# Kernel optimization log

Measured on AMD Instinct MI355X. Metric: run time of the kernel, lower is better.

The kernel has to match this reference:

```python
import jax, jax.numpy as jnp
import numpy as np

K = 4  # kNN neighbors


def build_edges(density_maps, k):
    B, _, H, W = density_maps.shape
    N = H * W
    flat = density_maps.reshape(B, N)
    # [B, N, N] pairwise absolute density distance
    dist = jnp.abs(flat[:, :, None] - flat[:, None, :])
    # k nearest (excluding self at position 0)
    tgt = jnp.argsort(dist, axis=2)[:, :, 1:k + 1]  # [B, N, k]
    src = jnp.broadcast_to(jnp.arange(N)[None, :, None], (B, N, k))
    offset = (jnp.arange(B) * N)[:, None, None]
    src = (src + offset).reshape(-1)
    tgt = (tgt + offset).reshape(-1)
    n_total = B * N
    loops = jnp.arange(n_total)
    row = jnp.concatenate([src, loops])  # source nodes
    col = jnp.concatenate([tgt, loops])  # target nodes
    return row, col, n_total


def gcn_conv(x, row, col, W, b, n_nodes):
    # symmetric deg^-1/2 normalization, deg computed on target (col)
    deg = jax.ops.segment_sum(jnp.ones_like(col, dtype=x.dtype), col, num_segments=n_nodes)
    dinv = jnp.where(deg > 0, jax.lax.rsqrt(deg), 0.0)
    norm = dinv[row] * dinv[col]  # [E]
    h = x @ W  # transform first, then propagate
    msg = norm[:, None] * h[row]
    out = jax.ops.segment_sum(msg, col, num_segments=n_nodes)
    return out + b


def setup_inputs() -> dict:
    key = jax.random.key(0)
    k1, k2, k3, k4, k5, k6 = jax.random.split(key, 6)
    B, Cin, Chid, Cout, H, W = 4, 256, 512, 256, 64, 64
    density_maps = jax.random.uniform(k1, (B, 1, H, W), dtype=jnp.float32)
    feature_maps = jax.random.normal(k2, (B, Cin, H, W), dtype=jnp.float32)
    W1 = jax.random.normal(k3, (Cin, Chid), dtype=jnp.float32) * (1.0 / np.sqrt(Cin))
    b1 = jnp.zeros((Chid,), dtype=jnp.float32)
    W2 = jax.random.normal(k4, (Chid, Cout), dtype=jnp.float32) * (1.0 / np.sqrt(Chid))
    b2 = jnp.zeros((Cout,), dtype=jnp.float32)
    return {"density_maps": density_maps, "feature_maps": feature_maps,
            "W1": W1, "b1": b1, "W2": W2, "b2": b2}


def reference(density_maps, feature_maps, W1, b1, W2, b2):
    B, Cin, H, Wd = feature_maps.shape
    row, col, n_total = build_edges(density_maps, K)
    # [B,C,H,W] -> [B*H*W, C] node features
    x = feature_maps.transpose(0, 2, 3, 1).reshape(-1, Cin)
    h = jax.nn.relu(gcn_conv(x, row, col, W1, b1, n_total))
    out = jax.nn.relu(gcn_conv(h, row, col, W2, b2, n_total))
    return out.reshape(B, H, Wd, -1).transpose(0, 3, 1, 2)
```

## Files before the change

### kernel.cpp

```cpp
#include <hip/hip_runtime.h>
#include <hip/hip_bf16.h>
#include <stdint.h>

#define N_NODES 16384
#define NPB     4096
#define NB      4
#define KNN     4
#define WIN     12
#define NBUK    4096

typedef short bf16x8 __attribute__((ext_vector_type(8)));
typedef float f32x4 __attribute__((ext_vector_type(4)));
typedef unsigned short u16x8 __attribute__((ext_vector_type(8)));

__device__ __forceinline__ unsigned short f2bf(float f) {
  unsigned u = __float_as_uint(f);
  unsigned r = (u + 0x7fff + ((u >> 16) & 1)) >> 16;
  return (unsigned short)r;
}
__device__ __forceinline__ float bf2f(unsigned short u) {
  return __uint_as_float(((unsigned)u) << 16);
}

__global__ __launch_bounds__(1024)
void bucket_kernel(const float* __restrict__ dm,
                   unsigned long long* __restrict__ skeys_g,
                   int* __restrict__ rank_g,
                   int* __restrict__ deg_g,
                   unsigned* __restrict__ mask_g) {
  __shared__ int sHist[4096];
  __shared__ int sCur[4096];
  __shared__ unsigned long long sKeys[4096];
  int* part1 = (int*)sKeys;
  int* part2 = (int*)(sKeys + 512);
  const int t = threadIdx.x, b = blockIdx.x;
  const float* d = dm + b * NPB;

  unsigned long long kv[4]; int bk[4];
#pragma unroll
  for (int r = 0; r < 4; ++r) sHist[t + r * 1024] = 0;
  __syncthreads();
#pragma unroll
  for (int r = 0; r < 4; ++r) {
    int i = t + r * 1024;
    float v = d[i];
    kv[r] = (((unsigned long long)__float_as_uint(v)) << 32) | (unsigned)i;
    int k = (int)(v * (float)NBUK); if (k > NBUK - 1) k = NBUK - 1;
    bk[r] = k;
    atomicAdd(&sHist[k], 1);
  }
  __syncthreads();
  int c0 = sHist[4 * t + 0], c1 = sHist[4 * t + 1];
  int c2 = sHist[4 * t + 2], c3 = sHist[4 * t + 3];
  part1[t] = c0 + c1 + c2 + c3;
  __syncthreads();
  if (t < 64) {
    int s = 0;
#pragma unroll
    for (int k = 0; k < 16; ++k) s += part1[16 * t + k];
    part2[t] = s;
  }
  __syncthreads();
  if (t == 0) {
    int a = 0;
    for (int u = 0; u < 64; ++u) { int v = part2[u]; part2[u] = a; a += v; }
  }
  __syncthreads();
  int base = part2[t >> 4];
  for (int k = (t >> 4) * 16; k < t; ++k) base += part1[k];
  sHist[4 * t + 0] = base; sCur[4 * t + 0] = base; base += c0;
  sHist[4 * t + 1] = base; sCur[4 * t + 1] = base; base += c1;
  sHist[4 * t + 2] = base; sCur[4 * t + 2] = base; base += c2;
  sHist[4 * t + 3] = base; sCur[4 * t + 3] = base;
  __syncthreads();
#pragma unroll
  for (int r = 0; r < 4; ++r) {
    int slot = atomicAdd(&sCur[bk[r]], 1);
    sKeys[slot] = kv[r];
  }
  __syncthreads();
#pragma unroll
  for (int r = 0; r < 4; ++r) {
    int g = t + r * 1024;
    int s0 = sHist[g];
    int s1 = (g == NPB - 1) ? NPB : sHist[g + 1];
    for (int i = s0 + 1; i < s1; ++i) {
      unsigned long long x = sKeys[i];
      int j = i - 1;
      while (j >= s0 && sKeys[j] > x) { sKeys[j + 1] = sKeys[j]; --j; }
      sKeys[j + 1] = x;
    }
  }
  __syncthreads();
#pragma unroll
  for (int r = 0; r < 4; ++r) {
    int i = t + r * 1024;
    unsigned long long k = sKeys[i];
    skeys_g[b * NPB + i] = k;
    rank_g[b * NPB + (int)(k & 0xffffffffull)] = i;
    deg_g[b * NPB + i] = 1;
    mask_g[b * NPB + i] = 0;
  }
}

__global__ void select_kernel(const unsigned long long* __restrict__ skeys,
                              int* __restrict__ deg, unsigned* __restrict__ mask) {
  int p = blockIdx.x * 256 + threadIdx.x;
  if (p >= N_NODES) return;
  int b = p >> 12, pl = p & (NPB - 1);
  const unsigned long long* sk = skeys + b * NPB;
  unsigned long long kp = sk[pl];
  float di = __uint_as_float((unsigned)(kp >> 32));
  int lo = pl - WIN; if (lo < 0) lo = 0;
  int hi = pl + WIN; if (hi > NPB - 1) hi = NPB - 1;
  unsigned long long k0 = ~0ull, k1 = ~0ull, k2 = ~0ull, k3 = ~0ull, k4 = ~0ull;
  for (int q = lo; q <= hi; ++q) {
    unsigned long long key = sk[q];
    float v = __uint_as_float((unsigned)(key >> 32));
    float dist = fabsf(di - v);
    unsigned long long dk = (((unsigned long long)__float_as_uint(dist)) << 24) |
                            ((key & 0xfffull) << 12) | (unsigned)q;
    if (dk < k4) {
      if (dk < k0)      { k4 = k3; k3 = k2; k2 = k1; k1 = k0; k0 = dk; }
      else if (dk < k1) { k4 = k3; k3 = k2; k2 = k1; k1 = dk; }
      else if (dk < k2) { k4 = k3; k3 = k2; k2 = dk; }
      else if (dk < k3) { k4 = k3; k3 = dk; }
      else              { k4 = dk; }
    }
  }
  int base = b * NPB;
  int t0 = (int)(k1 & 0xfff), t1 = (int)(k2 & 0xfff);
  int t2 = (int)(k3 & 0xfff), t3 = (int)(k4 & 0xfff);
  atomicAdd(&deg[base + t0], 1); atomicOr(&mask[base + t0], 1u << (pl - t0 + WIN));
  atomicAdd(&deg[base + t1], 1); atomicOr(&mask[base + t1], 1u << (pl - t1 + WIN));
  atomicAdd(&deg[base + t2], 1); atomicOr(&mask[base + t2], 1u << (pl - t2 + WIN));
  atomicAdd(&deg[base + t3], 1); atomicOr(&mask[base + t3], 1u << (pl - t3 + WIN));
}

__global__ void cvt_all_kernel(const float* __restrict__ fm, unsigned short* __restrict__ px0,
                               const float* __restrict__ W1, unsigned short* __restrict__ W1t,
                               const float* __restrict__ W2, unsigned short* __restrict__ W2t,
                               const int* __restrict__ rank) {
  __shared__ float tile[64][33];
  int z = blockIdx.z;
  const float* in; unsigned short* outbase; int Rin, Cin, r0, c0;
  bool perm = false;
  if (z < NB) {
    in = fm + (size_t)z * 256 * 4096; outbase = px0 + (size_t)z * NPB * 256;
    Rin = 256; Cin = 4096; perm = true;
    c0 = blockIdx.x * 32; r0 = blockIdx.y * 64;
  } else {
    int id = blockIdx.y * 128 + blockIdx.x;
    if (id < 64)       { in = W1; outbase = W1t; Rin = 256; Cin = 512; c0 = (id & 15) * 32; r0 = (id >> 4) * 64; }
    else if (id < 128) { id -= 64; in = W2; outbase = W2t; Rin = 512; Cin = 256; c0 = (id & 7) * 32; r0 = (id >> 3) * 64; }
    else return;
  }
  int tx = threadIdx.x & 31, ty = threadIdx.x >> 5;
  const float* ip = in + (size_t)(r0 + ty) * Cin + c0 + tx;
#pragma unroll
  for (int i = 0; i < 8; ++i) tile[ty + 8 * i][tx] = ip[(size_t)(8 * i) * Cin];
  __syncthreads();
  int orow = threadIdx.x >> 3;
  int oseg = (threadIdx.x & 7) * 8;
  int outrow = c0 + orow;
  if (perm) outrow = rank[(size_t)z * NPB + outrow];
  unsigned short* op = outbase + (size_t)outrow * Rin + r0 + oseg;
  u16x8 o;
#pragma unroll
  for (int k = 0; k < 8; ++k) o[k] = f2bf(tile[oseg + k][orow]);
  *(u16x8*)op = o;
}

__global__ __launch_bounds__(256)
void transpose64_kernel(const float* __restrict__ in, float* __restrict__ out) {
  __shared__ float tile[64][68];
  int cb = blockIdx.x * 64;
  int nb = blockIdx.y * 64;
  int b = blockIdx.z;
  int r = threadIdx.x >> 2, q = threadIdx.x & 3;
  const float* ip = in + ((size_t)b * NPB + nb + r) * 256 + cb;
#pragma unroll
  for (int it = 0; it < 4; ++it) {
    int c = q * 4 + it * 16;
    *(float4*)&tile[r][c] = *(const float4*)(ip + c);
  }
  __syncthreads();
  float* op = out + ((size_t)b * 256 + cb + r) * 4096 + nb;
#pragma unroll
  for (int it = 0; it < 4; ++it) {
    int n = q * 4 + it * 16;
    float4 v;
    v.x = tile[n + 0][r]; v.y = tile[n + 1][r];
    v.z = tile[n + 2][r]; v.w = tile[n + 3][r];
    *(float4*)(op + n) = v;
  }
}

__global__ void prop_kernel(const unsigned short* __restrict__ in,
                            unsigned short* __restrict__ out,
                            const unsigned* __restrict__ mask,
                            const int* __restrict__ deg) {
  int i = blockIdx.x * 8 + (threadIdx.x >> 5);
  int l = threadIdx.x & 31;
  unsigned m = mask[i];
  float a[8] = {};
#pragma unroll
  for (int off = 0; off < 2 * WIN + 1; ++off) {
    int c = ((m >> off) & 1) + (off == WIN);
    if (c) {
      int q = i + off - WIN;
      float dj = (float)c * rsqrtf((float)deg[q]);
      u16x8 u = *(const u16x8*)(in + (size_t)q * 256 + l * 8);
#pragma unroll
      for (int k = 0; k < 8; ++k) a[k] = fmaf(dj, bf2f(u[k]), a[k]);
    }
  }
  float di = rsqrtf((float)deg[i]);
  u16x8 o;
#pragma unroll
  for (int k = 0; k < 8; ++k) o[k] = f2bf(a[k] * di);
  *(u16x8*)(out + (size_t)i * 256 + l * 8) = o;
}

__global__ void prop2_kernel(const unsigned short* __restrict__ in,
                             float* __restrict__ out,
                             const unsigned* __restrict__ mask,
                             const int* __restrict__ deg,
                             const float* __restrict__ bias,
                             const unsigned long long* __restrict__ skeys) {
  int i = blockIdx.x * 8 + (threadIdx.x >> 5);
  int l = threadIdx.x & 31;
  unsigned m = mask[i];
  float a[8] = {};
#pragma unroll
  for (int off = 0; off < 2 * WIN + 1; ++off) {
    int c = ((m >> off) & 1) + (off == WIN);
    if (c) {
      int q = i + off - WIN;
      float dj = (float)c * rsqrtf((float)deg[q]);
      u16x8 u = *(const u16x8*)(in + (size_t)q * 256 + l * 8);
#pragma unroll
      for (int k = 0; k < 8; ++k) a[k] = fmaf(dj, bf2f(u[k]), a[k]);
    }
  }
  float di = rsqrtf((float)deg[i]);
  int node = (i & ~(NPB - 1)) + (int)(skeys[i] & 0xffffffffull);
  float4 o0, o1;
  o0.x = fmaxf(a[0] * di + bias[l * 8 + 0], 0.f);
  o0.y = fmaxf(a[1] * di + bias[l * 8 + 1], 0.f);
  o0.z = fmaxf(a[2] * di + bias[l * 8 + 2], 0.f);
  o0.w = fmaxf(a[3] * di + bias[l * 8 + 3], 0.f);
  o1.x = fmaxf(a[4] * di + bias[l * 8 + 4], 0.f);
  o1.y = fmaxf(a[5] * di + bias[l * 8 + 5], 0.f);
  o1.z = fmaxf(a[6] * di + bias[l * 8 + 6], 0.f);
  o1.w = fmaxf(a[7] * di + bias[l * 8 + 7], 0.f);
  *(float4*)(out + (size_t)node * 256 + l * 8) = o0;
  *(float4*)(out + (size_t)node * 256 + l * 8 + 4) = o1;
}

template <bool BIAS_RELU, bool OUT_BF16, int NI>
__global__ __launch_bounds__(256)
void gemm_bf16_kernel(const unsigned short* __restrict__ A,
                      const unsigned short* __restrict__ Bt,
                      void* __restrict__ C, const float* __restrict__ bias,
                      int M, int N, int K) {
  __shared__ char lds[8192 + NI * 8192];
  const int tid = threadIdx.x;
  const int l = tid & 63, w = tid >> 6;
  const int bm = blockIdx.x * 64, bn = blockIdx.y * (64 * NI);
  f32x4 acc[4][NI] = {};

  for (int k0 = 0; k0 < K; k0 += 64) {
    __syncthreads();
#pragma unroll
    for (int q = 0; q < 2; ++q) {
      int o = q * 4096 + tid * 16;
      int r = o >> 7;
      int gc = ((o >> 4) & 7) ^ (r & 7);
      const char* srcA = (const char*)A + ((size_t)(bm + r) * K + k0) * 2 + gc * 16;
      __builtin_amdgcn_global_load_lds(
          (const __attribute__((address_space(1))) void*)srcA,
          (__attribute__((address_space(3))) void*)(lds + o), 16, 0, 0);
    }
#pragma unroll
    for (int q = 0; q < 2 * NI; ++q) {
      int o = q * 4096 + tid * 16;
      int r = o >> 7;
      int gc = ((o >> 4) & 7) ^ (r & 7);
      const char* srcB = (const char*)Bt + ((size_t)(bn + r) * K + k0) * 2 + gc * 16;
      __builtin_amdgcn_global_load_lds(
          (const __attribute__((address_space(1))) void*)srcB,
          (__attribute__((address_space(3))) void*)(lds + 8192 + o), 16, 0, 0);
    }
    __syncthreads();

#pragma unroll
    for (int kk = 0; kk < 64; kk += 32) {
      bf16x8 af[4], bf[NI];
      int gc = (kk >> 3) + (l >> 4);
#pragma unroll
      for (int mi = 0; mi < 4; ++mi) {
        int r = mi * 16 + (l & 15);
        af[mi] = *(const bf16x8*)(lds + r * 128 + ((gc ^ (r & 7)) << 4));
      }
#pragma unroll
      for (int ni = 0; ni < NI; ++ni) {
        int r = w * (16 * NI) + ni * 16 + (l & 15);
        bf[ni] = *(const bf16x8*)(lds + 8192 + r * 128 + ((gc ^ (r & 7)) << 4));
      }
#pragma unroll
      for (int mi = 0; mi < 4; ++mi)
#pragma unroll
        for (int ni = 0; ni < NI; ++ni)
          acc[mi][ni] = __builtin_amdgcn_mfma_f32_16x16x32_bf16(af[mi], bf[ni],
                                                                acc[mi][ni], 0, 0, 0);
    }
  }

#pragma unroll
  for (int mi = 0; mi < 4; ++mi) {
#pragma unroll
    for (int ni = 0; ni < NI; ++ni) {
      int row0 = bm + mi * 16 + ((l >> 4) << 2);
      int col = bn + w * (16 * NI) + ni * 16 + (l & 15);
      float bv = BIAS_RELU ? bias[col] : 0.f;
      f32x4 v = acc[mi][ni];
#pragma unroll
      for (int r = 0; r < 4; ++r) {
        float val = v[r];
        if (BIAS_RELU) val = fmaxf(val + bv, 0.f);
        if (OUT_BF16)
          ((unsigned short*)C)[(size_t)(row0 + r) * N + col] = f2bf(val);
        else
          ((float*)C)[(size_t)(row0 + r) * N + col] = val;
      }
    }
  }
}

extern "C" void kernel_launch(void* const* d_in, const int* in_sizes, int n_in,
                              void* d_out, int out_size, void* d_ws, size_t ws_size,
                              hipStream_t stream) {
  const float* dm = (const float*)d_in[0];
  const float* fm = (const float*)d_in[1];
  const float* W1 = (const float*)d_in[2];
  const float* b1 = (const float*)d_in[3];
  const float* W2 = (const float*)d_in[4];
  const float* b2 = (const float*)d_in[5];
  float* out = (float*)d_out;

  char* ws = (char*)d_ws;
  int*                deg   = (int*)(ws + 0x040000);
  unsigned*           mask  = (unsigned*)(ws + 0x060000);
  unsigned long long* skeys = (unsigned long long*)(ws + 0x100000);
  int*                rank  = (int*)(ws + 0x130000);
  unsigned short*     W1t   = (unsigned short*)(ws + 0x190000);
  unsigned short*     W2t   = (unsigned short*)(ws + 0x1D0000);
  unsigned short*     px0   = (unsigned short*)(ws + 0x0400000);
  unsigned short*     px    = (unsigned short*)(ws + 0x0C00000);
  unsigned short*     h1    = (unsigned short*)(ws + 0x1400000);
  unsigned short*     t2    = (unsigned short*)(ws + 0x2400000);
  float*              xout  = (float*)(ws + 0x2C00000);
  (void)ws_size; (void)in_sizes; (void)n_in; (void)out_size;

  bucket_kernel<<<NB, 1024, 0, stream>>>(dm, skeys, rank, deg, mask);
  select_kernel<<<64, 256, 0, stream>>>(skeys, deg, mask);

  cvt_all_kernel<<<dim3(128, 4, NB + 1), 256, 0, stream>>>(fm, px0, W1, W1t, W2, W2t, rank);

  prop_kernel<<<N_NODES / 8, 256, 0, stream>>>(px0, px, mask, deg);
  gemm_bf16_kernel<true, true, 1><<<dim3(256, 8), 256, 0, stream>>>(
      px, W1t, h1, b1, 16384, 512, 256);

  gemm_bf16_kernel<false, true, 1><<<dim3(256, 4), 256, 0, stream>>>(
      h1, W2t, t2, nullptr, 16384, 256, 512);
  prop2_kernel<<<N_NODES / 8, 256, 0, stream>>>(t2, xout, mask, deg, b2, skeys);

  transpose64_kernel<<<dim3(4, 64, NB), 256, 0, stream>>>(xout, out);
}
```

Baseline: 76.50 us.

## Fuse kNN selection into conversion kernel and deepen GEMM K-tile to 256

Merges the kNN neighbor selection into the feature/weight conversion kernel, using spare blocks of the z=NB slice, which drops one kernel launch. The GEMM now stages a 256-wide K slab per iteration in 64KB of LDS instead of 64, so it needs fewer barriers and loop iterations. The cost is higher LDS use, which can limit occupancy, and no overlap of loads with compute within an iteration.

```diff
diff --git a/kernel.cpp b/kernel.cpp
--- a/kernel.cpp
+++ b/kernel.cpp
@@ -103,44 +103,12 @@
   }
 }
 
-__global__ void select_kernel(const unsigned long long* __restrict__ skeys,
+__global__ void cvtsel_kernel(const float* __restrict__ fm, unsigned short* __restrict__ px0,
+                              const float* __restrict__ W1, unsigned short* __restrict__ W1t,
+                              const float* __restrict__ W2, unsigned short* __restrict__ W2t,
+                              const int* __restrict__ rank,
+                              const unsigned long long* __restrict__ skeys,
                               int* __restrict__ deg, unsigned* __restrict__ mask) {
-  int p = blockIdx.x * 256 + threadIdx.x;
-  if (p >= N_NODES) return;
-  int b = p >> 12, pl = p & (NPB - 1);
-  const unsigned long long* sk = skeys + b * NPB;
-  unsigned long long kp = sk[pl];
-  float di = __uint_as_float((unsigned)(kp >> 32));
-  int lo = pl - WIN; if (lo < 0) lo = 0;
-  int hi = pl + WIN; if (hi > NPB - 1) hi = NPB - 1;
-  unsigned long long k0 = ~0ull, k1 = ~0ull, k2 = ~0ull, k3 = ~0ull, k4 = ~0ull;
-  for (int q = lo; q <= hi; ++q) {
-    unsigned long long key = sk[q];
-    float v = __uint_as_float((unsigned)(key >> 32));
-    float dist = fabsf(di - v);
-    unsigned long long dk = (((unsigned long long)__float_as_uint(dist)) << 24) |
-                            ((key & 0xfffull) << 12) | (unsigned)q;
-    if (dk < k4) {
-      if (dk < k0)      { k4 = k3; k3 = k2; k2 = k1; k1 = k0; k0 = dk; }
-      else if (dk < k1) { k4 = k3; k3 = k2; k2 = k1; k1 = dk; }
-      else if (dk < k2) { k4 = k3; k3 = k2; k2 = dk; }
-      else if (dk < k3) { k4 = k3; k3 = dk; }
-      else              { k4 = dk; }
-    }
-  }
-  int base = b * NPB;
-  int t0 = (int)(k1 & 0xfff), t1 = (int)(k2 & 0xfff);
-  int t2 = (int)(k3 & 0xfff), t3 = (int)(k4 & 0xfff);
-  atomicAdd(&deg[base + t0], 1); atomicOr(&mask[base + t0], 1u << (pl - t0 + WIN));
-  atomicAdd(&deg[base + t1], 1); atomicOr(&mask[base + t1], 1u << (pl - t1 + WIN));
-  atomicAdd(&deg[base + t2], 1); atomicOr(&mask[base + t2], 1u << (pl - t2 + WIN));
-  atomicAdd(&deg[base + t3], 1); atomicOr(&mask[base + t3], 1u << (pl - t3 + WIN));
-}
-
-__global__ void cvt_all_kernel(const float* __restrict__ fm, unsigned short* __restrict__ px0,
-                               const float* __restrict__ W1, unsigned short* __restrict__ W1t,
-                               const float* __restrict__ W2, unsigned short* __restrict__ W2t,
-                               const int* __restrict__ rank) {
   __shared__ float tile[64][33];
   int z = blockIdx.z;
   const float* in; unsigned short* outbase; int Rin, Cin, r0, c0;
@@ -151,8 +119,40 @@
     c0 = blockIdx.x * 32; r0 = blockIdx.y * 64;
   } else {
     int id = blockIdx.y * 128 + blockIdx.x;
-    if (id < 64)       { in = W1; outbase = W1t; Rin = 256; Cin = 512; c0 = (id & 15) * 32; r0 = (id >> 4) * 64; }
-    else if (id < 128) { id -= 64; in = W2; outbase = W2t; Rin = 512; Cin = 256; c0 = (id & 7) * 32; r0 = (id >> 3) * 64; }
+    if (id >= 128 && id < 192) {
+      int p = (id - 128) * 256 + threadIdx.x;
+      int b = p >> 12, pl = p & (NPB - 1);
+      const unsigned long long* sk = skeys + b * NPB;
+      unsigned long long kp = sk[pl];
+      float di = __uint_as_float((unsigned)(kp >> 32));
+      int lo = pl - WIN; if (lo < 0) lo = 0;
+      int hi = pl + WIN; if (hi > NPB - 1) hi = NPB - 1;
+      unsigned long long k0 = ~0ull, k1 = ~0ull, k2 = ~0ull, k3 = ~0ull, k4 = ~0ull;
+      for (int q = lo; q <= hi; ++q) {
+        unsigned long long key = sk[q];
+        float v = __uint_as_float((unsigned)(key >> 32));
+        float dist = fabsf(di - v);
+        unsigned long long dk = (((unsigned long long)__float_as_uint(dist)) << 24) |
+                                ((key & 0xfffull) << 12) | (unsigned)q;
+        if (dk < k4) {
+          if (dk < k0)      { k4 = k3; k3 = k2; k2 = k1; k1 = k0; k0 = dk; }
+          else if (dk < k1) { k4 = k3; k3 = k2; k2 = k1; k1 = dk; }
+          else if (dk < k2) { k4 = k3; k3 = k2; k2 = dk; }
+          else if (dk < k3) { k4 = k3; k3 = dk; }
+          else              { k4 = dk; }
+        }
+      }
+      int base = b * NPB;
+      int t0 = (int)(k1 & 0xfff), t1 = (int)(k2 & 0xfff);
+      int t2 = (int)(k3 & 0xfff), t3 = (int)(k4 & 0xfff);
+      atomicAdd(&deg[base + t0], 1); atomicOr(&mask[base + t0], 1u << (pl - t0 + WIN));
+      atomicAdd(&deg[base + t1], 1); atomicOr(&mask[base + t1], 1u << (pl - t1 + WIN));
+      atomicAdd(&deg[base + t2], 1); atomicOr(&mask[base + t2], 1u << (pl - t2 + WIN));
+      atomicAdd(&deg[base + t3], 1); atomicOr(&mask[base + t3], 1u << (pl - t3 + WIN));
+      return;
+    }
+    if (id >= 64 && id < 128) { id -= 64; in = W2; outbase = W2t; Rin = 512; Cin = 256; c0 = (id & 7) * 32; r0 = (id >> 3) * 64; }
+    else if (id < 64)         { in = W1; outbase = W1t; Rin = 256; Cin = 512; c0 = (id & 15) * 32; r0 = (id >> 4) * 64; }
     else return;
   }
   int tx = threadIdx.x & 31, ty = threadIdx.x >> 5;
@@ -258,82 +258,66 @@
   *(float4*)(out + (size_t)node * 256 + l * 8 + 4) = o1;
 }
 
-template <bool BIAS_RELU, bool OUT_BF16, int NI>
+template <bool BIAS_RELU>
 __global__ __launch_bounds__(256)
 void gemm_bf16_kernel(const unsigned short* __restrict__ A,
                       const unsigned short* __restrict__ Bt,
-                      void* __restrict__ C, const float* __restrict__ bias,
+                      unsigned short* __restrict__ C, const float* __restrict__ bias,
                       int M, int N, int K) {
-  __shared__ char lds[8192 + NI * 8192];
+  __shared__ char lds[65536];
   const int tid = threadIdx.x;
   const int l = tid & 63, w = tid >> 6;
-  const int bm = blockIdx.x * 64, bn = blockIdx.y * (64 * NI);
-  f32x4 acc[4][NI] = {};
-
-  for (int k0 = 0; k0 < K; k0 += 64) {
+  const int bm = blockIdx.x * 64, bn = blockIdx.y * 64;
+  f32x4 acc[4] = {};
+
+  for (int k0 = 0; k0 < K; k0 += 256) {
     __syncthreads();
 #pragma unroll
-    for (int q = 0; q < 2; ++q) {
+    for (int q = 0; q < 8; ++q) {
       int o = q * 4096 + tid * 16;
-      int r = o >> 7;
-      int gc = ((o >> 4) & 7) ^ (r & 7);
+      int r = o >> 9;
+      int gc = ((o >> 4) & 31) ^ (r & 7);
       const char* srcA = (const char*)A + ((size_t)(bm + r) * K + k0) * 2 + gc * 16;
       __builtin_amdgcn_global_load_lds(
           (const __attribute__((address_space(1))) void*)srcA,
           (__attribute__((address_space(3))) void*)(lds + o), 16, 0, 0);
-    }
-#pragma unroll
-    for (int q = 0; q < 2 * NI; ++q) {
-      int o = q * 4096 + tid * 16;
-      int r = o >> 7;
-      int gc = ((o >> 4) & 7) ^ (r & 7);
       const char* srcB = (const char*)Bt + ((size_t)(bn + r) * K + k0) * 2 + gc * 16;
       __builtin_amdgcn_global_load_lds(
           (const __attribute__((address_space(1))) void*)srcB,
-          (__attribute__((address_space(3))) void*)(lds + 8192 + o), 16, 0, 0);
+          (__attribute__((address_space(3))) void*)(lds + 32768 + o), 16, 0, 0);
     }
     __syncthreads();
 
 #pragma unroll
-    for (int kk = 0; kk < 64; kk += 32) {
-      bf16x8 af[4], bf[NI];
+    for (int kk = 0; kk < 256; kk += 32) {
+      bf16x8 af[4], bf;
       int gc = (kk >> 3) + (l >> 4);
 #pragma unroll
       for (int mi = 0; mi < 4; ++mi) {
         int r = mi * 16 + (l & 15);
-        af[mi] = *(const bf16x8*)(lds + r * 128 + ((gc ^ (r & 7)) << 4));
+        af[mi] = *(const bf16x8*)(lds + r * 512 + ((gc ^ (r & 7)) << 4));
       }
-#pragma unroll
-      for (int ni = 0; ni < NI; ++ni) {
-        int r = w * (16 * NI) + ni * 16 + (l & 15);
-        bf[ni] = *(const bf16x8*)(lds + 8192 + r * 128 + ((gc ^ (r & 7)) << 4));
+      {
+        int r = w * 16 + (l & 15);
+        bf = *(const bf16x8*)(lds + 32768 + r * 512 + ((gc ^ (r & 7)) << 4));
       }
 #pragma unroll
       for (int mi = 0; mi < 4; ++mi)
-#pragma unroll
-        for (int ni = 0; ni < NI; ++ni)
-          acc[mi][ni] = __builtin_amdgcn_mfma_f32_16x16x32_bf16(af[mi], bf[ni],
-                                                                acc[mi][ni], 0, 0, 0);
+        acc[mi] = __builtin_amdgcn_mfma_f32_16x16x32_bf16(af[mi], bf, acc[mi], 0, 0, 0);
     }
   }
 
 #pragma unroll
   for (int mi = 0; mi < 4; ++mi) {
-#pragma unroll
-    for (int ni = 0; ni < NI; ++ni) {
-      int row0 = bm + mi * 16 + ((l >> 4) << 2);
-      int col = bn + w * (16 * NI) + ni * 16 + (l & 15);
-      float bv = BIAS_RELU ? bias[col] : 0.f;
-      f32x4 v = acc[mi][ni];
-#pragma unroll
-      for (int r = 0; r < 4; ++r) {
-        float val = v[r];
-        if (BIAS_RELU) val = fmaxf(val + bv, 0.f);
-        if (OUT_BF16)
-          ((unsigned short*)C)[(size_t)(row0 + r) * N + col] = f2bf(val);
-        else
-          ((float*)C)[(size_t)(row0 + r) * N + col] = val;
-      }
+    int row0 = bm + mi * 16 + ((l >> 4) << 2);
+    int col = bn + w * 16 + (l & 15);
+    float bv = BIAS_RELU ? bias[col] : 0.f;
+    f32x4 v = acc[mi];
+#pragma unroll
+    for (int r = 0; r < 4; ++r) {
+      float val = v[r];
+      if (BIAS_RELU) val = fmaxf(val + bv, 0.f);
+      C[(size_t)(row0 + r) * N + col] = f2bf(val);
     }
   }
 }
@@ -364,15 +348,14 @@
   (void)ws_size; (void)in_sizes; (void)n_in; (void)out_size;
 
   bucket_kernel<<<NB, 1024, 0, stream>>>(dm, skeys, rank, deg, mask);
-  select_kernel<<<64, 256, 0, stream>>>(skeys, deg, mask);
-
-  cvt_all_kernel<<<dim3(128, 4, NB + 1), 256, 0, stream>>>(fm, px0, W1, W1t, W2, W2t, rank);
+  cvtsel_kernel<<<dim3(128, 4, NB + 1), 256, 0, stream>>>(
+      fm, px0, W1, W1t, W2, W2t, rank, skeys, deg, mask);
 
   prop_kernel<<<N_NODES / 8, 256, 0, stream>>>(px0, px, mask, deg);
-  gemm_bf16_kernel<true, true, 1><<<dim3(256, 8), 256, 0, stream>>>(
+  gemm_bf16_kernel<true><<<dim3(256, 8), 256, 0, stream>>>(
       px, W1t, h1, b1, 16384, 512, 256);
 
-  gemm_bf16_kernel<false, true, 1><<<dim3(256, 4), 256, 0, stream>>>(
+  gemm_bf16_kernel<false><<<dim3(256, 4), 256, 0, stream>>>(
       h1, W2t, t2, nullptr, 16384, 256, 512);
   prop2_kernel<<<N_NODES / 8, 256, 0, stream>>>(t2, xout, mask, deg, b2, skeys);
 
```

After: 79.00 us. 1.03x slower.
